# Performance work log

Hardware: AMD Instinct MI355X
Metric: run time of the kernel (lower is better)

The kernel has to match this reference:

```python
import jax, jax.numpy as jnp
import numpy as np

# NOTE: SoftAttn (not shown in source) is assumed to be a channel-wise softmax over the
# kernel_size**2 attention maps, as is standard in involution/dynamic-conv designs.

def conv2d(x, w, b=None, stride=1, pad=0, dil=1):
    y = jax.lax.conv_general_dilated(
        x, w, (stride, stride), [(pad, pad), (pad, pad)],
        rhs_dilation=(dil, dil), dimension_numbers=('NCHW', 'OIHW', 'NCHW'))
    return y if b is None else y + b[None, :, None, None]

def prelu(x, a):
    return jnp.where(x >= 0, x, a * x)

def pixel_shuffle(x, r):
    b, c, h, w = x.shape
    x = x.reshape(b, c // (r * r), r, r, h, w)
    x = x.transpose(0, 1, 4, 2, 5, 3)  # b, c', h, r, w, r
    return x.reshape(b, c // (r * r), h * r, w * r)

def aflb(x, aw, ab, fw):
    # Adaptive Fine-grained Local Block: per-position attention over k^2 taps,
    # broadcast across input channels, then contracted with the conv weight.
    k = 3
    C = x.shape[1]
    att = jax.nn.softmax(conv2d(x, aw, ab, pad=1), axis=1)  # [b, k*k, H, W]
    # unfold (channel-major, spatial-minor, matching torch F.unfold)
    p = jax.lax.conv_general_dilated_patches(
        x, (k, k), (1, 1), [(1, 1), (1, 1)],
        dimension_numbers=('NCHW', 'OIHW', 'NCHW'))  # [b, C*k*k, H, W]
    b_, _, H, W = p.shape
    p = p.reshape(b_, C, k * k, H, W)
    atx = p * att[:, None]  # broadcast attention over channels
    return jnp.einsum('bcphw,ocp->bohw', atx, fw.reshape(fw.shape[0], C, k * k))

def rmrs(x, wa, ba, wb, bb, wc, bc, awA, abA, fwA, awB, abB, fwB):
    o = jnp.concatenate([
        conv2d(x, wa, ba, pad=1),
        conv2d(x, wb, bb, pad=2, dil=2),
        conv2d(x, wc, bc, pad=3, dil=3)], axis=1)
    o = aflb(o, awA, abA, fwA)
    o = aflb(o, awB, abB, fwB)
    return jax.nn.relu(o + x)


def setup_inputs() -> dict:
    key = jax.random.key(0)
    ks = iter(jax.random.split(key, 64))
    def rn(shape, s=0.05):
        return jax.random.normal(next(ks), shape, jnp.float32) * s
    a = lambda: jnp.full((1,), 0.25, jnp.float32)
    d = dict(
        ms_up=rn((2, 4, 256, 256), 1.0),
        ms_org=rn((2, 4, 64, 64), 1.0),
        pan=rn((2, 1, 256, 256), 1.0),
        w_up4=rn((64, 4, 3, 3)), b_up4=jnp.zeros(64, jnp.float32), a_up4=a(),
        w_blk53=rn((30, 5, 3, 3)), b_blk53=jnp.zeros(30, jnp.float32), a_blk53=a(),
        w_blk43=rn((30, 4, 3, 3)), b_blk43=jnp.zeros(30, jnp.float32), a_blk43=a(),
        w1a=rn((20, 60, 3, 3)), b1a=jnp.zeros(20, jnp.float32),
        w1b=rn((20, 60, 3, 3)), b1b=jnp.zeros(20, jnp.float32),
        w1c=rn((20, 60, 3, 3)), b1c=jnp.zeros(20, jnp.float32),
        aw1=rn((9, 60, 3, 3)), ab1=jnp.zeros(9, jnp.float32), fw1=rn((60, 60, 3, 3)),
        aw2=rn((9, 60, 3, 3)), ab2=jnp.zeros(9, jnp.float32), fw2=rn((60, 60, 3, 3)),
        w_blk2=rn((30, 60, 3, 3)), b_blk2=jnp.zeros(30, jnp.float32), a_blk2=a(),
        w2a=rn((10, 30, 3, 3)), b2a=jnp.zeros(10, jnp.float32),
        w2b=rn((10, 30, 3, 3)), b2b=jnp.zeros(10, jnp.float32),
        w2c=rn((10, 30, 3, 3)), b2c=jnp.zeros(10, jnp.float32),
        aw3=rn((9, 30, 3, 3)), ab3=jnp.zeros(9, jnp.float32), fw3=rn((30, 30, 3, 3)),
        aw4=rn((9, 30, 3, 3)), ab4=jnp.zeros(9, jnp.float32), fw4=rn((30, 30, 3, 3)),
        w_c6=rn((4, 30, 3, 3)), b_c6=jnp.zeros(4, jnp.float32),
    )
    return d


def reference(ms_up, ms_org, pan,
              w_up4, b_up4, a_up4,
              w_blk53, b_blk53, a_blk53,
              w_blk43, b_blk43, a_blk43,
              w1a, b1a, w1b, b1b, w1c, b1c,
              aw1, ab1, fw1, aw2, ab2, fw2,
              w_blk2, b_blk2, a_blk2,
              w2a, b2a, w2b, b2b, w2c, b2c,
              aw3, ab3, fw3, aw4, ab4, fw4,
              w_c6, b_c6):
    ms_org_up = prelu(pixel_shuffle(conv2d(ms_org, w_up4, b_up4, pad=1), 4), a_up4)
    data1 = jnp.concatenate([ms_org_up, pan], axis=1)  # [b,5,H,W]
    pan_conv = prelu(conv2d(data1, w_blk53, b_blk53, pad=1), a_blk53)
    ms_up_conv = prelu(conv2d(ms_up, w_blk43, b_blk43, pad=1), a_blk43)
    out1 = jnp.concatenate([ms_up_conv, pan_conv], axis=1)  # [b,60,H,W]
    out2 = rmrs(out1, w1a, b1a, w1b, b1b, w1c, b1c, aw1, ab1, fw1, aw2, ab2, fw2)
    out3 = prelu(conv2d(out2, w_blk2, b_blk2, pad=1), a_blk2)  # [b,30,H,W]
    out3 = rmrs(out3, w2a, b2a, w2b, b2b, w2c, b2c, aw3, ab3, fw3, aw4, ab4, fw4)
    out8 = conv2d(out3, w_c6, b_c6, pad=1)
    return out8 + ms_up
```

## Files before the change

### kernel.cpp

```cpp
#include <hip/hip_runtime.h>

typedef __attribute__((ext_vector_type(8))) short short8;
typedef __attribute__((ext_vector_type(4))) float f32x4;
typedef __attribute__((ext_vector_type(4))) int i32x4;

#define HW 65536

__device__ __forceinline__ float bf2f(unsigned short u){
    union { unsigned int i; float f; } x; x.i = ((unsigned int)u) << 16; return x.f;
}
__device__ __forceinline__ unsigned short f2bf(float f){
    union { float f; unsigned int i; } x; x.f = f;
    unsigned int r = x.i + 0x7fffu + ((x.i >> 16) & 1u);
    return (unsigned short)(r >> 16);
}
__device__ __forceinline__ unsigned int pack2(float a, float b){
    return (unsigned int)f2bf(a) | ((unsigned int)f2bf(b) << 16);
}
__device__ __forceinline__ i32x4 addrelu4(i32x4 a, i32x4 b){
    i32x4 o;
#pragma unroll
    for (int k = 0; k < 4; ++k) {
        unsigned int ua = (unsigned int)a[k], ub = (unsigned int)b[k];
        float x0 = bf2f((unsigned short)(ua & 0xffff)) + bf2f((unsigned short)(ub & 0xffff));
        float x1 = bf2f((unsigned short)(ua >> 16))    + bf2f((unsigned short)(ub >> 16));
        o[k] = (int)(((unsigned int)f2bf(fmaxf(x0, 0.f))) |
                     ((unsigned int)f2bf(fmaxf(x1, 0.f)) << 16));
    }
    return o;
}

template<int KK, int PRELU>
__global__ __launch_bounds__(256, 4) void sconv_k(
    const unsigned short* __restrict__ in,
    const unsigned short* __restrict__ wfrag,
    const float* __restrict__ bias,
    const float* __restrict__ alphap,
    unsigned short* __restrict__ outb, int cpad, int coff)
{
    constexpr int CPIN = KK * 32, SGR = KK * 4, SGRP = SGR + 1, SPX = 66;
    constexpr int NSTGDW = 3 * SPX * SGRP * 4;
    constexpr int ODP = 20;
    constexpr int OUTOFF = NSTGDW;
    __shared__ __align__(16) unsigned int sm[NSTGDW + 64 * ODP];
    const int tid = threadIdx.x;
    const int lane = tid & 63, wv = tid >> 6;
    const int col = lane & 15, g = lane >> 4;
    const int bx = blockIdx.x;
    const int xcd = bx & 7, t = bx >> 3;
    const int y0 = xcd * 32 + (t & 31);
    const int x0 = ((t >> 5) & 3) * 64;
    const int b = blockIdx.z;
    const unsigned short* inb = in + (size_t)b * HW * CPIN;

#pragma unroll
    for (int rr = 0; rr < 3; ++rr) {
        const int yy = y0 + rr - 1;
        for (int u = tid; u < SPX * SGR; u += 256) {
            const int slot = u & (SGR - 1), px = u / SGR;
            const int xx = x0 - 1 + px;
            i32x4 v = {0,0,0,0};
            if ((unsigned)yy < 256u && (unsigned)xx < 256u)
                v = *(const i32x4*)(inb + (size_t)(yy * 256 + xx) * CPIN + slot * 8);
            *(i32x4*)&sm[((rr * SPX + px) * SGRP + slot) * 4] = v;
        }
    }
    if (tid < 64) sm[OUTOFF + tid * ODP + 15] = 0;
    __syncthreads();

    const short8* wp = (const short8*)wfrag;
    f32x4 acc[2];
    acc[0] = (f32x4){0.f,0.f,0.f,0.f}; acc[1] = (f32x4){0.f,0.f,0.f,0.f};
#pragma unroll
    for (int tap = 0; tap < 9; ++tap) {
        const int dy = tap / 3 - 1, dx = tap % 3 - 1;
        const int rl = dy + 1;
        short8 af[2][KK];
#pragma unroll
        for (int mt = 0; mt < 2; ++mt)
#pragma unroll
            for (int kk = 0; kk < KK; ++kk)
                af[mt][kk] = wp[((tap * 2 + mt) * KK + kk) * 64 + lane];
        const int pl = 1 + wv * 16 + col + dx;
#pragma unroll
        for (int kk = 0; kk < KK; ++kk) {
            short8 bf = *(const short8*)&sm[((rl * SPX + pl) * SGRP + kk * 4 + g) * 4];
#pragma unroll
            for (int mt = 0; mt < 2; ++mt)
                acc[mt] = __builtin_amdgcn_mfma_f32_16x16x32_bf16(af[mt][kk], bf, acc[mt], 0, 0, 0);
        }
    }
    const float al = PRELU ? __ldg(alphap) : 0.f;
    const int px = wv * 16 + col;
#pragma unroll
    for (int mt = 0; mt < 2; ++mt)
#pragma unroll
        for (int e = 0; e < 2; ++e) {
            const int rb = mt * 16 + g * 4 + e * 2;
            if (rb < 30) {
                float v0 = acc[mt][e * 2]     + __ldg(bias + rb);
                float v1 = acc[mt][e * 2 + 1] + ((rb + 1 < 30) ? __ldg(bias + rb + 1) : 0.f);
                if (PRELU) { v0 = v0 >= 0.f ? v0 : al * v0; v1 = v1 >= 0.f ? v1 : al * v1; }
                if (rb + 1 >= 30) v1 = 0.f;
                sm[OUTOFF + px * ODP + (rb >> 1)] = pack2(v0, v1);
            }
        }
    __syncthreads();
    {
        const int slot = tid & 3, opx = tid >> 2;
        i32x4 v = *(i32x4*)&sm[OUTOFF + opx * ODP + slot * 4];
        const size_t go = ((size_t)b * HW + (size_t)y0 * 256 + x0 + opx) * cpad + coff + slot * 8;
        *(i32x4*)(outb + go) = v;
    }
}

template<int KK, int MR>
__global__ __launch_bounds__(256, 4) void trident_s(
    const unsigned short* __restrict__ in,
    const unsigned short* __restrict__ wf0, const unsigned short* __restrict__ wf1,
    const unsigned short* __restrict__ wf2,
    const float* __restrict__ b0, const float* __restrict__ b1, const float* __restrict__ b2,
    unsigned short* __restrict__ outb)
{
    constexpr int CPIN = KK * 32, CPAD = KK * 32;
    constexpr int SGR = KK * 4, SGRP = SGR + 1, SPX = 70;
    constexpr int MT_ = (KK == 2) ? 2 : 1;
    constexpr int CPP = KK * 4, ODP = (CPP + 1) * 4;
    constexpr int NSTGDW = 3 * SPX * SGRP * 4;
    constexpr int OUTOFF = NSTGDW;
    __shared__ __align__(16) unsigned int sm[NSTGDW + 64 * ODP];
    const int tid = threadIdx.x;
    const int lane = tid & 63, wv = tid >> 6;
    const int col = lane & 15, g = lane >> 4;
    const int bx = blockIdx.x;
    const int xcd = bx & 7, t = bx >> 3;
    const int y0 = xcd * 32 + (t & 31);
    const int x0 = ((t >> 5) & 3) * 64;
    const int b = blockIdx.z;
    const unsigned short* inb = in + (size_t)b * HW * CPIN;

    auto stage_row = [&](int srow, int yy) {
        for (int u = tid; u < SPX * SGR; u += 256) {
            const int slot = u & (SGR - 1), px = u / SGR;
            const int xx = x0 - 3 + px;
            i32x4 v = {0,0,0,0};
            if ((unsigned)yy < 256u && (unsigned)xx < 256u)
                v = *(const i32x4*)(inb + (size_t)(yy * 256 + xx) * CPIN + slot * 8);
            *(i32x4*)&sm[((srow * SPX + px) * SGRP + slot) * 4] = v;
        }
    };

    const unsigned short* wfs[3] = {wf0, wf1, wf2};
    const float* bss[3] = {b0, b1, b2};

    stage_row(0, y0); stage_row(1, y0 - 1); stage_row(2, y0 + 1);
    if (tid < 64) {
#pragma unroll
        for (int dwp = 3 * MR / 2; dwp < CPP * 4; ++dwp) sm[OUTOFF + tid * ODP + dwp] = 0;
    }
    __syncthreads();

#pragma unroll
    for (int which = 0; which < 3; ++which) {
        const int d = which + 1;
        const short8* wp = (const short8*)wfs[which];
        const float* bs = bss[which];
        f32x4 acc[MT_];
#pragma unroll
        for (int mt = 0; mt < MT_; ++mt) acc[mt] = (f32x4){0.f,0.f,0.f,0.f};
#pragma unroll
        for (int tap = 0; tap < 9; ++tap) {
            const int dy = tap / 3 - 1, dx = tap % 3 - 1;
            const int rl = (dy == 0) ? 0 : (dy < 0 ? 1 : 2);
            short8 af[MT_][KK];
#pragma unroll
            for (int mt = 0; mt < MT_; ++mt)
#pragma unroll
                for (int kk = 0; kk < KK; ++kk)
                    af[mt][kk] = wp[((tap * MT_ + mt) * KK + kk) * 64 + lane];
            const int pl = 3 + wv * 16 + col + dx * d;
#pragma unroll
            for (int kk = 0; kk < KK; ++kk) {
                short8 bf = *(const short8*)&sm[((rl * SPX + pl) * SGRP + kk * 4 + g) * 4];
#pragma unroll
                for (int mt = 0; mt < MT_; ++mt)
                    acc[mt] = __builtin_amdgcn_mfma_f32_16x16x32_bf16(af[mt][kk], bf, acc[mt], 0, 0, 0);
            }
        }
        const int px = wv * 16 + col;
#pragma unroll
        for (int mt = 0; mt < MT_; ++mt)
#pragma unroll
            for (int e = 0; e < 2; ++e) {
                const int rb = mt * 16 + g * 4 + e * 2;
                if (rb < MR) {
                    float v0 = acc[mt][e * 2]     + __ldg(bs + rb);
                    float v1 = acc[mt][e * 2 + 1] + ((rb + 1 < MR) ? __ldg(bs + rb + 1) : 0.f);
                    if (rb + 1 >= MR) v1 = 0.f;
                    sm[OUTOFF + px * ODP + ((which * MR + rb) >> 1)] = pack2(v0, v1);
                }
            }
        __syncthreads();
        if (which < 2) {
            stage_row(1, y0 - (d + 1)); stage_row(2, y0 + (d + 1));
            __syncthreads();
        }
    }

    for (int u = tid; u < 64 * CPP; u += 256) {
        const int slot = u & (CPP - 1), opx = u / CPP;
        i32x4 v = *(i32x4*)&sm[OUTOFF + opx * ODP + slot * 4];
        const size_t go = ((size_t)b * HW + (size_t)y0 * 256 + x0 + opx) * CPAD + slot * 8;
        *(i32x4*)(outb + go) = v;
    }
}

template<int KK, int RPB, int RES>
__global__ __launch_bounds__(256, 4) void aflb_p(
    const unsigned short* __restrict__ in,
    const unsigned short* __restrict__ awf, const float* __restrict__ ab,
    const unsigned short* __restrict__ fwf,
    const unsigned short* __restrict__ res,
    unsigned short* __restrict__ outb)
{
    constexpr int CPIN = KK * 32, MTT = 2 * KK, CPAD = 16 * MTT;
    constexpr int SROWS = RPB + 2, SPX = 66, SGR = KK * 4, SGRP = SGR + 1;
    constexpr int CPP = CPAD / 8, ODP = (CPP + 1) * 4;
    constexpr int NSTGDW = SROWS * SPX * SGRP * 4;
    constexpr int ATOFF = NSTGDW;
    constexpr int NATT = RPB * 64 * 9;
    constexpr int OUTOFF = ATOFF + NATT;
    __shared__ __align__(16) unsigned int sm[OUTOFF + RPB * 64 * ODP];

    const int tid = threadIdx.x;
    const int lane = tid & 63, wv = tid >> 6;
    const int col = lane & 15, g = lane >> 4;
    const int bx = blockIdx.x;
    const int xcd = bx & 7, t = bx >> 3;
    const int y0 = (RPB == 1) ? (xcd * 32 + (t & 31)) : (xcd * 32 + (t & 15) * 2);
    const int xseg = (RPB == 1) ? ((t >> 5) & 3) : ((t >> 4) & 3);
    const int x0 = xseg * 64;
    const int b = blockIdx.z;
    const unsigned short* inb = in + (size_t)b * HW * CPIN;

    for (int u = tid; u < SROWS * SPX * SGR; u += 256) {
        const int slot = u & (SGR - 1);
        const int px = (u / SGR) % SPX;
        const int row = u / (SGR * SPX);
        const int yy = y0 + row - 1, xx = x0 - 1 + px;
        i32x4 v = {0,0,0,0};
        if ((unsigned)yy < 256u && (unsigned)xx < 256u)
            v = *(const i32x4*)(inb + (size_t)(yy * 256 + xx) * CPIN + slot * 8);
        *(i32x4*)&sm[((row * SPX + px) * SGRP + slot) * 4] = v;
    }
    __syncthreads();

    const short8* awp = (const short8*)awf;
    const short8* fwp = (const short8*)fwf;

    constexpr int NF1 = (RPB == 1) ? 1 : 2;
    const int arow = (RPB == 1) ? 0 : (wv >> 1);
    const int apx0 = (RPB == 1) ? (wv * 16) : ((wv & 1) * 32);
    f32x4 aacc[NF1];
#pragma unroll
    for (int nf = 0; nf < NF1; ++nf) aacc[nf] = (f32x4){0.f,0.f,0.f,0.f};
#pragma unroll
    for (int tap = 0; tap < 9; ++tap) {
        const int dy = tap / 3 - 1, dx = tap % 3 - 1;
        const int rl = arow + dy + 1;
        short8 afa[KK];
#pragma unroll
        for (int kk = 0; kk < KK; ++kk)
            afa[kk] = awp[(tap * KK + kk) * 64 + lane];
#pragma unroll
        for (int nf = 0; nf < NF1; ++nf) {
            const int pl = 1 + apx0 + nf * 16 + col + dx;
#pragma unroll
            for (int kk = 0; kk < KK; ++kk) {
                short8 bf = *(const short8*)&sm[((rl * SPX + pl) * SGRP + kk * 4 + g) * 4];
                aacc[nf] = __builtin_amdgcn_mfma_f32_16x16x32_bf16(afa[kk], bf, aacc[nf], 0, 0, 0);
            }
        }
    }
#pragma unroll
    for (int nf = 0; nf < NF1; ++nf) {
        float v[4];
        float m = -1e30f;
#pragma unroll
        for (int r = 0; r < 4; ++r) {
            const int row = g * 4 + r;
            v[r] = (row < 9) ? (aacc[nf][r] + __ldg(ab + row)) : -1e30f;
            m = fmaxf(m, v[r]);
        }
        m = fmaxf(m, __shfl_xor(m, 16));
        m = fmaxf(m, __shfl_xor(m, 32));
        float e[4]; float s = 0.f;
#pragma unroll
        for (int r = 0; r < 4; ++r) { e[r] = (g * 4 + r < 9) ? __expf(v[r] - m) : 0.f; s += e[r]; }
        s += __shfl_xor(s, 16);
        s += __shfl_xor(s, 32);
        const float inv = 1.f / s;
        const int px = apx0 + nf * 16 + col;
#pragma unroll
        for (int r = 0; r < 4; ++r) {
            const int row = g * 4 + r;
            if (row < 9) sm[ATOFF + (arow * 64 + px) * 9 + row] = __float_as_uint(e[r] * inv);
        }
    }
    __syncthreads();

    const int prow = (RPB == 1) ? 0 : (wv >> 1);
    const int mt = (RPB == 1) ? wv : (wv & 1);
    f32x4 acc[4];
#pragma unroll
    for (int nf = 0; nf < 4; ++nf) acc[nf] = (f32x4){0.f,0.f,0.f,0.f};
#pragma unroll
    for (int tap = 0; tap < 9; ++tap) {
        const int dy = tap / 3 - 1, dx = tap % 3 - 1;
        const int rl = prow + dy + 1;
        float av[4];
#pragma unroll
        for (int nf = 0; nf < 4; ++nf)
            av[nf] = __uint_as_float(sm[ATOFF + (prow * 64 + nf * 16 + col) * 9 + tap]);
        short8 af[KK];
#pragma unroll
        for (int kk = 0; kk < KK; ++kk)
            af[kk] = fwp[((tap * MTT + mt) * KK + kk) * 64 + lane];
#pragma unroll
        for (int nf = 0; nf < 4; ++nf) {
            const int pl = 1 + nf * 16 + col + dx;
            f32x4 p = (f32x4){0.f,0.f,0.f,0.f};
#pragma unroll
            for (int kk = 0; kk < KK; ++kk) {
                short8 bf = *(const short8*)&sm[((rl * SPX + pl) * SGRP + kk * 4 + g) * 4];
                p = __builtin_amdgcn_mfma_f32_16x16x32_bf16(af[kk], bf, p, 0, 0, 0);
            }
#pragma unroll
            for (int r = 0; r < 4; ++r)
                acc[nf][r] = fmaf(av[nf], p[r], acc[nf][r]);
        }
    }
    __syncthreads();

#pragma unroll
    for (int nf = 0; nf < 4; ++nf) {
        const int px = nf * 16 + col;
        const int base = OUTOFF + ((RPB == 2 ? prow * 64 : 0) + px) * ODP;
        const int rp = mt * 8 + g * 2;
        unsigned long long w =
            (unsigned long long)pack2(acc[nf][0], acc[nf][1]) |
            ((unsigned long long)pack2(acc[nf][2], acc[nf][3]) << 32);
        *(unsigned long long*)&sm[base + rp] = w;
    }
    __syncthreads();

    constexpr int NOUT = RPB * 64 * CPP;
    for (int u = tid; u < NOUT; u += 256) {
        const int slot = u & (CPP - 1);
        const int px = (u / CPP) & 63;
        const int r = (RPB == 2) ? (u / (CPP * 64)) : 0;
        i32x4 v = *(i32x4*)&sm[OUTOFF + ((r * 64 + px) * ODP) + slot * 4];
        const size_t go = ((size_t)b * HW + (size_t)(y0 + r) * 256 + x0 + px) * CPAD + slot * 8;
        if (RES) v = addrelu4(v, *(const i32x4*)(res + go));
        *(i32x4*)(outb + go) = v;
    }
}

__global__ __launch_bounds__(256, 4) void final_k(
    const unsigned short* __restrict__ in,
    const unsigned short* __restrict__ wfrag,
    const float* __restrict__ bias,
    const float* __restrict__ msup, float* __restrict__ outf)
{
    constexpr int CPIN = 32, NF = 2;
    const int lane = threadIdx.x & 63, wv = threadIdx.x >> 6;
    const int col = lane & 15, g = lane >> 4;
    const int bx = blockIdx.x;
    const int xcd = bx & 7, t = bx >> 3;
    const int y = xcd * 32 + (t & 31);
    const int xh = t >> 5;
    const int b = blockIdx.z;
    const int x0 = xh * 128 + wv * 32;

    const unsigned short* inb = in + (size_t)b * HW * CPIN;
    const short8 kz = {0,0,0,0,0,0,0,0};
    const short8* wp = (const short8*)wfrag;

    f32x4 acc[NF];
#pragma unroll
    for (int nf = 0; nf < NF; ++nf) acc[nf] = (f32x4){0.f,0.f,0.f,0.f};
#pragma unroll
    for (int tap = 0; tap < 9; ++tap) {
        const int dy = tap / 3 - 1, dx = tap % 3 - 1;
        const int yy = y + dy;
        const bool yok = (unsigned)yy < 256u;
        const short8 af = wp[tap * 64 + lane];
#pragma unroll
        for (int nf = 0; nf < NF; ++nf) {
            const int xx = x0 + nf * 16 + col + dx;
            const bool ok = yok && ((unsigned)xx < 256u);
            const int pix = ok ? (yy * 256 + xx) : 0;
            short8 bf = *(const short8*)(inb + (size_t)pix * CPIN + g * 8);
            if (!ok) bf = kz;
            acc[nf] = __builtin_amdgcn_mfma_f32_16x16x32_bf16(af, bf, acc[nf], 0, 0, 0);
        }
    }
#pragma unroll
    for (int nf = 0; nf < NF; ++nf) {
        const int pix = y * 256 + x0 + nf * 16 + col;
        if (g == 0) {
#pragma unroll
            for (int r = 0; r < 4; ++r) {
                const size_t oi = ((size_t)b * 4 + r) * HW + pix;
                outf[oi] = acc[nf][r] + __ldg(bias + r) + msup[oi];
            }
        }
    }
}

struct PrepDesc { const float* src; int cout, cin, kksh, mtsh, flags, dstoff, n; };
struct PrepArgs { PrepDesc d[18]; };

__global__ __launch_bounds__(256) void prep_k(PrepArgs pa, unsigned short* __restrict__ wb)
{
    const PrepDesc d = pa.d[blockIdx.y];
    const int e = blockIdx.x * 256 + threadIdx.x;
    if (e >= d.n) return;
    const int j = e & 7;
    const int lane = (e >> 3) & 63;
    const int i512 = e >> 9;
    const int kk = i512 & ((1 << d.kksh) - 1);
    const int mt = (i512 >> d.kksh) & ((1 << d.mtsh) - 1);
    const int tap = i512 >> (d.kksh + d.mtsh);
    const int rpos = mt * 16 + (lane & 15);
    const int kpos = kk * 32 + (lane >> 4) * 8 + j;
    int o = rpos, ic = kpos;
    bool ok = true;
    if (d.flags & 2) {
        if (rpos < 30) o = rpos;
        else if (rpos >= 32 && rpos < 62) o = rpos - 2;
        else ok = false;
    }
    if (d.flags & 1) {
        if (kpos < 30) ic = kpos;
        else if (kpos >= 32 && kpos < 62) ic = kpos - 2;
        else ok = false;
    }
    float v = 0.f;
    if (ok && o < d.cout && ic < d.cin) v = d.src[(o * d.cin + ic) * 9 + tap];
    wb[d.dstoff + e] = f2bf(v);
}

template<int CIN, int COUT, int OCB, int H, int W>
__launch_bounds__(256)
__global__ void upconv_k(const float* __restrict__ in, const float* __restrict__ wgt,
                         const float* __restrict__ bias, float* __restrict__ out)
{
    constexpr int HWp = H * W;
    constexpr int NOCB = COUT / OCB;
    const int tx = threadIdx.x;
    const int lx = tx & 63, ly = tx >> 6;
    const int gx = blockIdx.x * 64 + lx;
    const int gy = blockIdx.y * 4 + ly;
    const int b = blockIdx.z / NOCB;
    const int ocb = blockIdx.z % NOCB;
    const int pixp = gy * W + gx;
    const float* inb = in + (size_t)b * CIN * HWp;

    int off[9]; float mul[9];
#pragma unroll
    for (int dy = 0; dy < 3; ++dy)
#pragma unroll
        for (int dx = 0; dx < 3; ++dx) {
            int p = dy * 3 + dx;
            int yy = gy + dy - 1, xx = gx + dx - 1;
            bool okp = ((unsigned)yy < (unsigned)H) && ((unsigned)xx < (unsigned)W);
            off[p] = okp ? (yy * W + xx) : 0;
            mul[p] = okp ? 1.f : 0.f;
        }
    float acc[OCB];
#pragma unroll
    for (int o = 0; o < OCB; ++o) acc[o] = 0.f;
    const float* wbase = wgt + (size_t)(ocb * OCB) * CIN * 9;
#pragma unroll
    for (int ic = 0; ic < CIN; ++ic) {
        const float* ip = inb + (size_t)ic * HWp;
        float tv[9];
#pragma unroll
        for (int p = 0; p < 9; ++p) tv[p] = __ldg(ip + off[p]) * mul[p];
#pragma unroll
        for (int o = 0; o < OCB; ++o) {
            const float* wq = wbase + (size_t)(o * CIN + ic) * 9;
#pragma unroll
            for (int p = 0; p < 9; ++p) acc[o] = fmaf(tv[p], wq[p], acc[o]);
        }
    }
#pragma unroll
    for (int o = 0; o < OCB; ++o)
        out[((size_t)b * COUT + ocb * OCB + o) * HWp + pixp] = acc[o] + __ldg(bias + ocb * OCB + o);
}

__global__ __launch_bounds__(256) void build_inputs(
    const float* __restrict__ tup, const float* __restrict__ pan,
    const float* __restrict__ aup, const float* __restrict__ msup,
    unsigned short* __restrict__ data1, unsigned short* __restrict__ msb)
{
    const int i = blockIdx.x * 256 + threadIdx.x;
    const int b = i >> 16, pixp = i & 65535;
    const int y = pixp >> 8, x = pixp & 255;
    unsigned short o[32];
#pragma unroll
    for (int c = 0; c < 32; ++c) o[c] = 0;
    unsigned short* dst;
    if (blockIdx.y == 0) {
        const float a = __ldg(aup);
#pragma unroll
        for (int c = 0; c < 4; ++c) {
            const int ch = c * 16 + (y & 3) * 4 + (x & 3);
            float v = tup[(((size_t)b * 64 + ch) << 12) + ((y >> 2) << 6) + (x >> 2)];
            v = (v >= 0.f) ? v : a * v;
            o[c] = f2bf(v);
        }
        o[4] = f2bf(pan[((size_t)b << 16) + pixp]);
        dst = data1;
    } else {
#pragma unroll
        for (int c = 0; c < 4; ++c)
            o[c] = f2bf(msup[(((size_t)b * 4 + c) << 16) + pixp]);
        dst = msb;
    }
    short8* dp = (short8*)(dst + (size_t)i * 32);
#pragma unroll
    for (int q = 0; q < 4; ++q) {
        short8 s;
#pragma unroll
        for (int r = 0; r < 8; ++r) s[r] = (short)o[q * 8 + r];
        dp[q] = s;
    }
}

extern "C" void kernel_launch(void* const* d_in, const int* in_sizes, int n_in,
                              void* d_out, int out_size, void* d_ws, size_t ws_size,
                              hipStream_t stream) {
    const float* ms_up  = (const float*)d_in[0];
    const float* ms_org = (const float*)d_in[1];
    const float* pan    = (const float*)d_in[2];
    const float* w_up4  = (const float*)d_in[3];
    const float* b_up4  = (const float*)d_in[4];
    const float* a_up4  = (const float*)d_in[5];
    const float* w_blk53= (const float*)d_in[6];
    const float* b_blk53= (const float*)d_in[7];
    const float* a_blk53= (const float*)d_in[8];
    const float* w_blk43= (const float*)d_in[9];
    const float* b_blk43= (const float*)d_in[10];
    const float* a_blk43= (const float*)d_in[11];
    const float* w1a=(const float*)d_in[12]; const float* b1a=(const float*)d_in[13];
    const float* w1b=(const float*)d_in[14]; const float* b1b=(const float*)d_in[15];
    const float* w1c=(const float*)d_in[16]; const float* b1c=(const float*)d_in[17];
    const float* aw1=(const float*)d_in[18]; const float* ab1=(const float*)d_in[19];
    const float* fw1=(const float*)d_in[20];
    const float* aw2=(const float*)d_in[21]; const float* ab2=(const float*)d_in[22];
    const float* fw2=(const float*)d_in[23];
    const float* w_blk2=(const float*)d_in[24]; const float* b_blk2=(const float*)d_in[25]; const float* a_blk2=(const float*)d_in[26];
    const float* w2a=(const float*)d_in[27]; const float* b2a=(const float*)d_in[28];
    const float* w2b=(const float*)d_in[29]; const float* b2b=(const float*)d_in[30];
    const float* w2c=(const float*)d_in[31]; const float* b2c=(const float*)d_in[32];
    const float* aw3=(const float*)d_in[33]; const float* ab3=(const float*)d_in[34];
    const float* fw3=(const float*)d_in[35];
    const float* aw4=(const float*)d_in[36]; const float* ab4=(const float*)d_in[37];
    const float* fw4=(const float*)d_in[38];
    const float* w_c6=(const float*)d_in[39]; const float* b_c6=(const float*)d_in[40];

    float* out = (float*)d_out;
    char* ws = (char*)d_ws;

    const size_t BIG = (size_t)2 * HW * 64 * 2;
    const size_t HALF = BIG / 2;
    unsigned short* bufA = (unsigned short*)(ws);
    unsigned short* bufB = (unsigned short*)(ws + BIG);
    unsigned short* bufC = (unsigned short*)(ws + 2 * BIG);
    unsigned short* data1 = bufC;
    float*          t_up  = (float*)(ws + 2 * BIG + HALF);
    unsigned short* msb   = bufB;
    unsigned short* bufD = bufC;
    unsigned short* bufE = bufB;
    unsigned short* bufF = bufA;
    unsigned short* wb = (unsigned short*)(ws + 3 * BIG);

    if (ws_size < 3 * BIG + 1000000) return;

    PrepArgs pa;
    int off = 0, li = 0;
    auto add = [&](const float* s, int cout, int cin, int mtsh, int kksh, int flags) {
        const int n = 9 << (mtsh + kksh + 9);
        pa.d[li].src = s; pa.d[li].cout = cout; pa.d[li].cin = cin;
        pa.d[li].kksh = kksh; pa.d[li].mtsh = mtsh; pa.d[li].flags = flags;
        pa.d[li].dstoff = off; pa.d[li].n = n;
        int ret = off; off += n; ++li; return ret;
    };
    const int o_blk43 = add(w_blk43, 30, 4, 1, 0, 0);
    const int o_blk53 = add(w_blk53, 30, 5, 1, 0, 0);
    const int o_w1a   = add(w1a, 20, 60, 1, 1, 1);
    const int o_w1b   = add(w1b, 20, 60, 1, 1, 1);
    const int o_w1c   = add(w1c, 20, 60, 1, 1, 1);
    const int o_aw1   = add(aw1,  9, 60, 0, 1, 0);
    const int o_fw1   = add(fw1, 60, 60, 2, 1, 0);
    const int o_aw2   = add(aw2,  9, 60, 0, 1, 0);
    const int o_fw2   = add(fw2, 60, 60, 2, 1, 2);
    const int o_blk2  = add(w_blk2, 30, 60, 1, 1, 1);
    const int o_w2a   = add(w2a, 10, 30, 0, 0, 0);
    const int o_w2b   = add(w2b, 10, 30, 0, 0, 0);
    const int o_w2c   = add(w2c, 10, 30, 0, 0, 0);
    const int o_aw3   = add(aw3,  9, 30, 0, 0, 0);
    const int o_fw3   = add(fw3, 30, 30, 1, 0, 0);
    const int o_aw4   = add(aw4,  9, 30, 0, 0, 0);
    const int o_fw4   = add(fw4, 30, 30, 1, 0, 0);
    const int o_c6    = add(w_c6,  4, 30, 0, 0, 0);

    prep_k<<<dim3(144, 18), 256, 0, stream>>>(pa, wb);

    upconv_k<4, 64, 16, 64, 64><<<dim3(1, 16, 8), 256, 0, stream>>>(ms_org, w_up4, b_up4, t_up);
    build_inputs<<<dim3(512, 2), 256, 0, stream>>>(t_up, pan, a_up4, ms_up, data1, msb);

    const dim3 B256(256);
    const dim3 G1(1024, 1, 2);
    const dim3 GH(512, 1, 2);

    sconv_k<1,1><<<G1,B256,0,stream>>>(msb,   wb+o_blk43, b_blk43, a_blk43, bufA, 64, 0);
    sconv_k<1,1><<<G1,B256,0,stream>>>(data1, wb+o_blk53, b_blk53, a_blk53, bufA, 64, 32);

    trident_s<2,20><<<G1,B256,0,stream>>>(bufA, wb+o_w1a, wb+o_w1b, wb+o_w1c, b1a, b1b, b1c, bufB);
    aflb_p<2,1,0><<<G1,B256,0,stream>>>(bufB, wb+o_aw1, ab1, wb+o_fw1, nullptr, bufC);
    aflb_p<2,1,1><<<G1,B256,0,stream>>>(bufC, wb+o_aw2, ab2, wb+o_fw2, bufA,   bufB);

    sconv_k<2,1><<<G1,B256,0,stream>>>(bufB, wb+o_blk2, b_blk2, a_blk2, bufD, 32, 0);

    trident_s<1,10><<<G1,B256,0,stream>>>(bufD, wb+o_w2a, wb+o_w2b, wb+o_w2c, b2a, b2b, b2c, bufE);
    aflb_p<1,2,0><<<GH,B256,0,stream>>>(bufE, wb+o_aw3, ab3, wb+o_fw3, nullptr, bufF);
    aflb_p<1,2,1><<<GH,B256,0,stream>>>(bufF, wb+o_aw4, ab4, wb+o_fw4, bufD,   bufE);

    final_k<<<GH,B256,0,stream>>>(bufE, wb+o_c6, b_c6, ms_up, out);
}
```

Baseline: 210.5 us.

## Prefetch next dilation's halo rows into registers during trident conv

The trident kernel now loads the two halo rows needed for the next dilation into registers before the current dilation's MFMA loop runs. Afterwards it writes them to shared memory, so global-load latency overlaps with compute instead of stalling between stages. This costs extra VGPRs for the prefetch buffer, which may hurt occupancy under the 256x4 launch bounds.

```diff
diff --git a/kernel.cpp b/kernel.cpp
--- a/kernel.cpp
+++ b/kernel.cpp
@@ -128,6 +128,8 @@
     constexpr int CPP = KK * 4, ODP = (CPP + 1) * 4;
     constexpr int NSTGDW = 3 * SPX * SGRP * 4;
     constexpr int OUTOFF = NSTGDW;
+    constexpr int NG1 = SPX * SGR;
+    constexpr int NIT2 = (2 * NG1 + 255) / 256;
     __shared__ __align__(16) unsigned int sm[NSTGDW + 64 * ODP];
     const int tid = threadIdx.x;
     const int lane = tid & 63, wv = tid >> 6;
@@ -140,7 +142,7 @@
     const unsigned short* inb = in + (size_t)b * HW * CPIN;
 
     auto stage_row = [&](int srow, int yy) {
-        for (int u = tid; u < SPX * SGR; u += 256) {
+        for (int u = tid; u < NG1; u += 256) {
             const int slot = u & (SGR - 1), px = u / SGR;
             const int xx = x0 - 3 + px;
             i32x4 v = {0,0,0,0};
@@ -149,22 +151,38 @@
             *(i32x4*)&sm[((srow * SPX + px) * SGRP + slot) * 4] = v;
         }
     };
-
-    const unsigned short* wfs[3] = {wf0, wf1, wf2};
-    const float* bss[3] = {b0, b1, b2};
-
-    stage_row(0, y0); stage_row(1, y0 - 1); stage_row(2, y0 + 1);
-    if (tid < 64) {
-#pragma unroll
-        for (int dwp = 3 * MR / 2; dwp < CPP * 4; ++dwp) sm[OUTOFF + tid * ODP + dwp] = 0;
-    }
-    __syncthreads();
-
-#pragma unroll
-    for (int which = 0; which < 3; ++which) {
-        const int d = which + 1;
-        const short8* wp = (const short8*)wfs[which];
-        const float* bs = bss[which];
+    i32x4 Rp[NIT2];
+    auto issue_pair = [&](int d) {
+#pragma unroll
+        for (int it = 0; it < NIT2; ++it) {
+            const int u = tid + it * 256;
+            i32x4 v = {0,0,0,0};
+            if (u < 2 * NG1) {
+                const int r = (u >= NG1) ? 1 : 0;
+                const int uu = u - r * NG1;
+                const int slot = uu & (SGR - 1), px = uu / SGR;
+                const int yy = y0 + (r ? d : -d);
+                const int xx = x0 - 3 + px;
+                if ((unsigned)yy < 256u && (unsigned)xx < 256u)
+                    v = *(const i32x4*)(inb + (size_t)(yy * 256 + xx) * CPIN + slot * 8);
+            }
+            Rp[it] = v;
+        }
+    };
+    auto write_pair = [&]() {
+#pragma unroll
+        for (int it = 0; it < NIT2; ++it) {
+            const int u = tid + it * 256;
+            if (u < 2 * NG1) {
+                const int r = (u >= NG1) ? 1 : 0;
+                const int uu = u - r * NG1;
+                const int slot = uu & (SGR - 1), px = uu / SGR;
+                *(i32x4*)&sm[(((1 + r) * SPX + px) * SGRP + slot) * 4] = Rp[it];
+            }
+        }
+    };
+    auto do_conv = [&](int d, const unsigned short* wfx, const float* bs, int which) {
+        const short8* wp = (const short8*)wfx;
         f32x4 acc[MT_];
 #pragma unroll
         for (int mt = 0; mt < MT_; ++mt) acc[mt] = (f32x4){0.f,0.f,0.f,0.f};
@@ -200,12 +218,29 @@
                     sm[OUTOFF + px * ODP + ((which * MR + rb) >> 1)] = pack2(v0, v1);
                 }
             }
-        __syncthreads();
-        if (which < 2) {
-            stage_row(1, y0 - (d + 1)); stage_row(2, y0 + (d + 1));
-            __syncthreads();
-        }
-    }
+    };
+
+    stage_row(0, y0); stage_row(1, y0 - 1); stage_row(2, y0 + 1);
+    issue_pair(2);
+    if (tid < 64) {
+#pragma unroll
+        for (int dwp = 3 * MR / 2; dwp < CPP * 4; ++dwp) sm[OUTOFF + tid * ODP + dwp] = 0;
+    }
+    __syncthreads();
+
+    do_conv(1, wf0, b0, 0);
+    __syncthreads();
+    write_pair();
+    issue_pair(3);
+    __syncthreads();
+
+    do_conv(2, wf1, b1, 1);
+    __syncthreads();
+    write_pair();
+    __syncthreads();
+
+    do_conv(3, wf2, b2, 2);
+    __syncthreads();
 
     for (int u = tid; u < 64 * CPP; u += 256) {
         const int slot = u & (CPP - 1), opx = u / CPP;
```

Result: no change. 206.5 us (-1.9%).

## Run trident dilation branches concurrently across waves with seven-row staging

Applied to the files above, without the earlier changes.

The trident kernel now stages all seven input rows once instead of restaging rows between dilation branches. Blocks grow to 384 threads so each pair of waves handles one dilation branch, and each wave covers 32 pixels with two MFMA tiles. This removes two restage-and-barrier rounds and serialized branch loops. In exchange it uses more LDS per block and lowers the occupancy bound from 4 blocks to 3.

```diff
diff --git a/kernel.cpp b/kernel.cpp
--- a/kernel.cpp
+++ b/kernel.cpp
@@ -115,7 +115,7 @@
 }
 
 template<int KK, int MR>
-__global__ __launch_bounds__(256, 4) void trident_s(
+__global__ __launch_bounds__(384, 3) void trident_w(
     const unsigned short* __restrict__ in,
     const unsigned short* __restrict__ wf0, const unsigned short* __restrict__ wf1,
     const unsigned short* __restrict__ wf2,
@@ -123,10 +123,10 @@
     unsigned short* __restrict__ outb)
 {
     constexpr int CPIN = KK * 32, CPAD = KK * 32;
-    constexpr int SGR = KK * 4, SGRP = SGR + 1, SPX = 70;
+    constexpr int SGR = KK * 4, SGRP = SGR + 1, SPX = 70, SROWS = 7;
     constexpr int MT_ = (KK == 2) ? 2 : 1;
     constexpr int CPP = KK * 4, ODP = (CPP + 1) * 4;
-    constexpr int NSTGDW = 3 * SPX * SGRP * 4;
+    constexpr int NSTGDW = SROWS * SPX * SGRP * 4;
     constexpr int OUTOFF = NSTGDW;
     __shared__ __align__(16) unsigned int sm[NSTGDW + 64 * ODP];
     const int tid = threadIdx.x;
@@ -139,75 +139,74 @@
     const int b = blockIdx.z;
     const unsigned short* inb = in + (size_t)b * HW * CPIN;
 
-    auto stage_row = [&](int srow, int yy) {
-        for (int u = tid; u < SPX * SGR; u += 256) {
-            const int slot = u & (SGR - 1), px = u / SGR;
-            const int xx = x0 - 3 + px;
-            i32x4 v = {0,0,0,0};
-            if ((unsigned)yy < 256u && (unsigned)xx < 256u)
-                v = *(const i32x4*)(inb + (size_t)(yy * 256 + xx) * CPIN + slot * 8);
-            *(i32x4*)&sm[((srow * SPX + px) * SGRP + slot) * 4] = v;
-        }
-    };
-
-    const unsigned short* wfs[3] = {wf0, wf1, wf2};
-    const float* bss[3] = {b0, b1, b2};
-
-    stage_row(0, y0); stage_row(1, y0 - 1); stage_row(2, y0 + 1);
+    for (int u = tid; u < SROWS * SPX * SGR; u += 384) {
+        const int slot = u & (SGR - 1);
+        const int px = (u / SGR) % SPX;
+        const int row = u / (SGR * SPX);
+        const int yy = y0 + row - 3, xx = x0 - 3 + px;
+        i32x4 v = {0,0,0,0};
+        if ((unsigned)yy < 256u && (unsigned)xx < 256u)
+            v = *(const i32x4*)(inb + (size_t)(yy * 256 + xx) * CPIN + slot * 8);
+        *(i32x4*)&sm[((row * SPX + px) * SGRP + slot) * 4] = v;
+    }
     if (tid < 64) {
 #pragma unroll
         for (int dwp = 3 * MR / 2; dwp < CPP * 4; ++dwp) sm[OUTOFF + tid * ODP + dwp] = 0;
     }
     __syncthreads();
 
-#pragma unroll
-    for (int which = 0; which < 3; ++which) {
-        const int d = which + 1;
-        const short8* wp = (const short8*)wfs[which];
-        const float* bs = bss[which];
-        f32x4 acc[MT_];
-#pragma unroll
-        for (int mt = 0; mt < MT_; ++mt) acc[mt] = (f32x4){0.f,0.f,0.f,0.f};
-#pragma unroll
-        for (int tap = 0; tap < 9; ++tap) {
-            const int dy = tap / 3 - 1, dx = tap % 3 - 1;
-            const int rl = (dy == 0) ? 0 : (dy < 0 ? 1 : 2);
-            short8 af[MT_][KK];
-#pragma unroll
-            for (int mt = 0; mt < MT_; ++mt)
-#pragma unroll
-                for (int kk = 0; kk < KK; ++kk)
-                    af[mt][kk] = wp[((tap * MT_ + mt) * KK + kk) * 64 + lane];
-            const int pl = 3 + wv * 16 + col + dx * d;
+    const int dil = wv >> 1, d = dil + 1, xh = wv & 1;
+    const unsigned short* wfx = (dil == 0) ? wf0 : ((dil == 1) ? wf1 : wf2);
+    const float* bs = (dil == 0) ? b0 : ((dil == 1) ? b1 : b2);
+    const short8* wp = (const short8*)wfx;
+
+    f32x4 acc[MT_][2];
+#pragma unroll
+    for (int mt = 0; mt < MT_; ++mt)
+#pragma unroll
+        for (int nf = 0; nf < 2; ++nf) acc[mt][nf] = (f32x4){0.f,0.f,0.f,0.f};
+
+#pragma unroll
+    for (int tap = 0; tap < 9; ++tap) {
+        const int dy = tap / 3 - 1, dx = tap % 3 - 1;
+        const int rl = 3 + dy * d;
+        short8 af[MT_][KK];
+#pragma unroll
+        for (int mt = 0; mt < MT_; ++mt)
+#pragma unroll
+            for (int kk = 0; kk < KK; ++kk)
+                af[mt][kk] = wp[((tap * MT_ + mt) * KK + kk) * 64 + lane];
+#pragma unroll
+        for (int nf = 0; nf < 2; ++nf) {
+            const int pl = 3 + xh * 32 + nf * 16 + col + dx * d;
 #pragma unroll
             for (int kk = 0; kk < KK; ++kk) {
                 short8 bf = *(const short8*)&sm[((rl * SPX + pl) * SGRP + kk * 4 + g) * 4];
 #pragma unroll
                 for (int mt = 0; mt < MT_; ++mt)
-                    acc[mt] = __builtin_amdgcn_mfma_f32_16x16x32_bf16(af[mt][kk], bf, acc[mt], 0, 0, 0);
+                    acc[mt][nf] = __builtin_amdgcn_mfma_f32_16x16x32_bf16(af[mt][kk], bf, acc[mt][nf], 0, 0, 0);
             }
         }
-        const int px = wv * 16 + col;
-#pragma unroll
-        for (int mt = 0; mt < MT_; ++mt)
+    }
+
+#pragma unroll
+    for (int mt = 0; mt < MT_; ++mt)
+#pragma unroll
+        for (int nf = 0; nf < 2; ++nf)
 #pragma unroll
             for (int e = 0; e < 2; ++e) {
                 const int rb = mt * 16 + g * 4 + e * 2;
                 if (rb < MR) {
-                    float v0 = acc[mt][e * 2]     + __ldg(bs + rb);
-                    float v1 = acc[mt][e * 2 + 1] + ((rb + 1 < MR) ? __ldg(bs + rb + 1) : 0.f);
+                    float v0 = acc[mt][nf][e * 2]     + __ldg(bs + rb);
+                    float v1 = acc[mt][nf][e * 2 + 1] + ((rb + 1 < MR) ? __ldg(bs + rb + 1) : 0.f);
                     if (rb + 1 >= MR) v1 = 0.f;
-                    sm[OUTOFF + px * ODP + ((which * MR + rb) >> 1)] = pack2(v0, v1);
+                    const int px = xh * 32 + nf * 16 + col;
+                    sm[OUTOFF + px * ODP + ((dil * MR + rb) >> 1)] = pack2(v0, v1);
                 }
             }
-        __syncthreads();
-        if (which < 2) {
-            stage_row(1, y0 - (d + 1)); stage_row(2, y0 + (d + 1));
-            __syncthreads();
-        }
-    }
-
-    for (int u = tid; u < 64 * CPP; u += 256) {
+    __syncthreads();
+
+    for (int u = tid; u < 64 * CPP; u += 384) {
         const int slot = u & (CPP - 1), opx = u / CPP;
         i32x4 v = *(i32x4*)&sm[OUTOFF + opx * ODP + slot * 4];
         const size_t go = ((size_t)b * HW + (size_t)y0 * 256 + x0 + opx) * CPAD + slot * 8;
@@ -622,20 +621,20 @@
     upconv_k<4, 64, 16, 64, 64><<<dim3(1, 16, 8), 256, 0, stream>>>(ms_org, w_up4, b_up4, t_up);
     build_inputs<<<dim3(512, 2), 256, 0, stream>>>(t_up, pan, a_up4, ms_up, data1, msb);
 
-    const dim3 B256(256);
+    const dim3 B256(256), B384(384);
     const dim3 G1(1024, 1, 2);
     const dim3 GH(512, 1, 2);
 
     sconv_k<1,1><<<G1,B256,0,stream>>>(msb,   wb+o_blk43, b_blk43, a_blk43, bufA, 64, 0);
     sconv_k<1,1><<<G1,B256,0,stream>>>(data1, wb+o_blk53, b_blk53, a_blk53, bufA, 64, 32);
 
-    trident_s<2,20><<<G1,B256,0,stream>>>(bufA, wb+o_w1a, wb+o_w1b, wb+o_w1c, b1a, b1b, b1c, bufB);
+    trident_w<2,20><<<G1,B384,0,stream>>>(bufA, wb+o_w1a, wb+o_w1b, wb+o_w1c, b1a, b1b, b1c, bufB);
     aflb_p<2,1,0><<<G1,B256,0,stream>>>(bufB, wb+o_aw1, ab1, wb+o_fw1, nullptr, bufC);
     aflb_p<2,1,1><<<G1,B256,0,stream>>>(bufC, wb+o_aw2, ab2, wb+o_fw2, bufA,   bufB);
 
     sconv_k<2,1><<<G1,B256,0,stream>>>(bufB, wb+o_blk2, b_blk2, a_blk2, bufD, 32, 0);
 
-    trident_s<1,10><<<G1,B256,0,stream>>>(bufD, wb+o_w2a, wb+o_w2b, wb+o_w2c, b2a, b2b, b2c, bufE);
+    trident_w<1,10><<<G1,B384,0,stream>>>(bufD, wb+o_w2a, wb+o_w2b, wb+o_w2c, b2a, b2b, b2c, bufE);
     aflb_p<1,2,0><<<GH,B256,0,stream>>>(bufE, wb+o_aw3, ab3, wb+o_fw3, nullptr, bufF);
     aflb_p<1,2,1><<<GH,B256,0,stream>>>(bufF, wb+o_aw4, ab4, wb+o_fw4, bufD,   bufE);
 
```

Result: slower. 221.7 us (+5.3%).
